# Optimization experiments

Measured on AMD Instinct MI355X. Metric: run time of the kernel, lower is better.

## Reference

```python
import jax, jax.numpy as jnp
import numpy as np

B, N, CI, CO, K = 4, 4096, 32, 32, 3


def setup_inputs() -> dict:
    key = jax.random.key(0)
    ks = jax.random.split(key, 28)
    f32 = jnp.float32

    def g(k, shape, scale=1.0):
        return jax.random.normal(k, shape, dtype=f32) * scale

    X = g(ks[0], (B, N, CI))
    L = g(ks[1], (N, N), 1.0 / np.sqrt(N))  # scaled Laplacian surrogate
    H = g(ks[2], (B, N, CO))
    C = g(ks[3], (B, N, CO))

    def conv_params(kw, ci):
        s = (2.0 / (ci + CO)) ** 0.5  # glorot-ish
        return g(kw, (K, ci, CO), s), jnp.zeros((CO,), f32)

    Wxi, bxi = conv_params(ks[4], CI)
    Whi, bhi = conv_params(ks[5], CO)
    Wxf, bxf = conv_params(ks[6], CI)
    Whf, bhf = conv_params(ks[7], CO)
    Wxc, bxc = conv_params(ks[8], CI)
    Whc, bhc = conv_params(ks[9], CO)
    Wxo, bxo = conv_params(ks[10], CI)
    Who, bho = conv_params(ks[11], CO)

    gs = (2.0 / (1 + CO)) ** 0.5
    w_ci = g(ks[12], (1, CO), gs)
    w_cf = g(ks[13], (1, CO), gs)
    w_co = g(ks[14], (1, CO), gs)
    b_i = jnp.zeros((1, CO), f32)
    b_f = jnp.zeros((1, CO), f32)
    b_c = jnp.zeros((1, CO), f32)
    b_o = jnp.zeros((1, CO), f32)

    return dict(X=X, L=L, H=H, C=C,
                Wxi=Wxi, bxi=bxi, Whi=Whi, bhi=bhi,
                Wxf=Wxf, bxf=bxf, Whf=Whf, bhf=bhf,
                Wxc=Wxc, bxc=bxc, Whc=Whc, bhc=bhc,
                Wxo=Wxo, bxo=bxo, Who=Who, bho=bho,
                w_ci=w_ci, w_cf=w_cf, w_co=w_co,
                b_i=b_i, b_f=b_f, b_c=b_c, b_o=b_o)


def cheb_conv(x, L, W, b):
    """Chebyshev graph conv: sum_k T_k(L) @ x @ W[k] + b.
    x: [B,N,F_in], L: [N,N], W: [K,F_in,F_out]."""
    Tx_prev = x                                    # T_0 = x
    out = jnp.einsum('bnf,fo->bno', Tx_prev, W[0])
    if W.shape[0] > 1:
        Tx = jnp.einsum('nm,bmf->bnf', L, x)       # T_1 = L x
        out = out + jnp.einsum('bnf,fo->bno', Tx, W[1])
        for k in range(2, W.shape[0]):
            Tx, Tx_prev = 2.0 * jnp.einsum('nm,bmf->bnf', L, Tx) - Tx_prev, Tx
            out = out + jnp.einsum('bnf,fo->bno', Tx, W[k])
    return out + b


def reference(X, L, H, C,
              Wxi, bxi, Whi, bhi,
              Wxf, bxf, Whf, bhf,
              Wxc, bxc, Whc, bhc,
              Wxo, bxo, Who, bho,
              w_ci, w_cf, w_co, b_i, b_f, b_c, b_o):
    I = jax.nn.sigmoid(cheb_conv(X, L, Wxi, bxi) + cheb_conv(H, L, Whi, bhi)
                       + w_ci * C + b_i)
    F = jax.nn.sigmoid(cheb_conv(X, L, Wxf, bxf) + cheb_conv(H, L, Whf, bhf)
                       + w_cf * C + b_f)
    T = jnp.tanh(cheb_conv(X, L, Wxc, bxc) + cheb_conv(H, L, Whc, bhc) + b_c)
    C_new = F * C + I * T
    O = jax.nn.sigmoid(cheb_conv(X, L, Wxo, bxo) + cheb_conv(H, L, Who, bho)
                       + w_co * C_new + b_o)
    H_new = O * jnp.tanh(C_new)
    return H_new, C_new
```

## Files before the change

### kernel.cpp

```cpp
#include <hip/hip_runtime.h>


typedef __bf16 bf16x8 __attribute__((ext_vector_type(8)));
typedef float f32x4 __attribute__((ext_vector_type(4)));

typedef unsigned short u16;
typedef unsigned int u32;

__device__ __forceinline__ float b2f(u16 h) {
  u32 u = ((u32)h) << 16;
  return __builtin_bit_cast(float, u);
}
__device__ __forceinline__ u16 f2b(float f) {
  u32 u = __builtin_bit_cast(u32, f);
  u += 0x7fffu + ((u >> 16) & 1u);
  return (u16)(u >> 16);
}
__device__ __forceinline__ u16 scrub16(u16 h) {
  return ((u16)(h & 0x7fffu) > (u16)0x7f80u) ? (u16)0 : h;
}
__device__ __forceinline__ float scrubf(float f) { return (f == f) ? f : 0.0f; }
__device__ __forceinline__ float sigm(float x) { return 1.0f / (1.0f + __expf(-x)); }
__device__ __forceinline__ float tanh_f(float x) { return 1.0f - 2.0f / (__expf(2.0f * x) + 1.0f); }

#define AS1 __attribute__((address_space(1)))
#define AS3 __attribute__((address_space(3)))
__device__ __forceinline__ void ld_lds16(const void* g, void* l) {
  __builtin_amdgcn_global_load_lds((const AS1 void*)g, (AS3 void*)l, 16, 0, 0);
}

#define FWS_M0T   0u
#define FWS_Y1T   2097152u
#define FWS_Y1N   4194304u
#define FWS_WCAT  6291456u
#define FWS_GB    6340608u
#define FWS_WC    6341120u
#define FWS_FLAG  6341632u
#define FWS_LBF   8388608u
#define FWS_PART  41943040u
#define FWS_TOTAL 58720256u
#define BWS_M0T   0u
#define BWS_Y1T   2097152u
#define BWS_Y1N   4194304u
#define BWS_T2N   6291456u
#define BWS_WCAT  8388608u
#define BWS_GB    8437760u
#define BWS_WC    8438272u
#define BWS_FLAG  8438784u

__global__ __launch_bounds__(64) void flag_k(const u16* __restrict__ L,
                                             u32* __restrict__ flag) {
  __shared__ int cnt;
  if (threadIdx.x == 0) cnt = 0;
  __syncthreads();
  int c = 0;
  for (int i = threadIdx.x; i < 1024; i += 64) {
    int e = (L[i] >> 7) & 0xFF;
    if (e >= 96 && e <= 126) ++c;
  }
  atomicAdd(&cnt, c);
  __syncthreads();
  if (threadIdx.x == 0) *flag = (cnt < 870) ? 1u : 0u;
}

__global__ __launch_bounds__(256) void convL_k(const void* __restrict__ L,
                                               u16* __restrict__ Lbf,
                                               const u32* __restrict__ flag) {
  const u32 mode = *flag;
  const int gtid = blockIdx.x * 256 + threadIdx.x;
  #pragma unroll
  for (int it = 0; it < 8; ++it) {
    const size_t e0 = ((size_t)it * 524288 + gtid) * 4;
    if (mode) {
      f32x4 v = *(const f32x4*)((const float*)L + e0);
      u16 o[4] = {f2b(v[0]), f2b(v[1]), f2b(v[2]), f2b(v[3])};
      *(uint2*)(Lbf + e0) = *(const uint2*)o;
    } else {
      *(uint2*)(Lbf + e0) = *(const uint2*)((const u16*)L + e0);
    }
  }
}

struct PackArgs {
  const void* in[27];
  u16* m0t;
  u16* wcat;
  float* gb;
  float* wc;
  const u32* flag;
};

__device__ __forceinline__ float rd_elem(const void* p, size_t idx, u32 mode) {
  return mode ? ((const float*)p)[idx] : b2f(((const u16*)p)[idx]);
}

__global__ __launch_bounds__(256) void pack_k(PackArgs pa) {
  const int bid = blockIdx.x;
  const int t = threadIdx.x;
  const u32 mode = *pa.flag;
  __shared__ u32 lds[256][17];

  if (bid < 128) {
    const int ts = bid >> 4, nc = bid & 15;
    const int xh = ts >> 2, b = ts & 3;
    const void* src = pa.in[xh ? 2 : 0];
    const int node = nc * 256 + t;
    const size_t rbase = ((size_t)b * 4096 + node) * 32;
    if (mode) {
      const f32x4* s4 = (const f32x4*)((const float*)src + rbase);
      u16 tv[32];
      #pragma unroll
      for (int j = 0; j < 8; ++j) {
        f32x4 v = s4[j];
        tv[j * 4] = f2b(v[0]); tv[j * 4 + 1] = f2b(v[1]);
        tv[j * 4 + 2] = f2b(v[2]); tv[j * 4 + 3] = f2b(v[3]);
      }
      #pragma unroll
      for (int i = 0; i < 16; ++i)
        lds[t][i] = (u32)tv[2 * i] | ((u32)tv[2 * i + 1] << 16);
    } else {
      const uint4* s4 = (const uint4*)((const u16*)src + rbase);
      uint4 q0 = s4[0], q1 = s4[1], q2 = s4[2], q3 = s4[3];
      lds[t][0] = q0.x;  lds[t][1] = q0.y;  lds[t][2] = q0.z;  lds[t][3] = q0.w;
      lds[t][4] = q1.x;  lds[t][5] = q1.y;  lds[t][6] = q1.z;  lds[t][7] = q1.w;
      lds[t][8] = q2.x;  lds[t][9] = q2.y;  lds[t][10] = q2.z; lds[t][11] = q2.w;
      lds[t][12] = q3.x; lds[t][13] = q3.y; lds[t][14] = q3.z; lds[t][15] = q3.w;
    }
    __syncthreads();
    const int f = t & 31, sc = t >> 5;
    const int ccol = xh * 128 + b * 32 + f;
    u16 tmp[32];
    #pragma unroll
    for (int i = 0; i < 32; ++i) {
      u32 wv = lds[sc * 32 + i][f >> 1];
      tmp[i] = scrub16((f & 1) ? (u16)(wv >> 16) : (u16)(wv & 0xffffu));
    }
    u16* dst = pa.m0t + (size_t)ccol * 4096 + nc * 256 + sc * 32;
    #pragma unroll
    for (int i = 0; i < 32; i += 8)
      *(uint4*)&dst[i] = *(const uint4*)&tmp[i];
  } else if (bid < 224) {
    const int wxi[4] = {4, 8, 12, 16};
    const int whi[4] = {6, 10, 14, 18};
    const int e = (bid - 128) * 256 + t;
    const int col = e / 192, j = e % 192;
    const int g = col >> 5, o = col & 31;
    const int a = j >> 5, jj = j & 31;
    const void* Wsrc = (a < 3) ? pa.in[wxi[g]] : pa.in[whi[g]];
    const int k = (a < 3) ? a : (a - 3);
    pa.wcat[e] = scrub16(f2b(rd_elem(Wsrc, k * 1024 + jj * 32 + o, mode)));
  } else {
    if (t < 128) {
      const int bx[4] = {5, 9, 13, 17}, bh[4] = {7, 11, 15, 19}, bb[4] = {23, 24, 25, 26};
      int g = t >> 5, o = t & 31;
      pa.gb[t] = scrubf(rd_elem(pa.in[bx[g]], o, mode) + rd_elem(pa.in[bh[g]], o, mode) +
                        rd_elem(pa.in[bb[g]], o, mode));
    } else if (t < 224) {
      int j = t - 128;
      int which = j >> 5, o = j & 31;
      pa.wc[j] = scrubf(rd_elem(pa.in[20 + which], o, mode));
    }
  }
}

__global__ __launch_bounds__(256, 4) void gemm_k(const u16* __restrict__ A,
                                                 const u16* __restrict__ B,
                                                 float* __restrict__ P) {
  __shared__ __align__(16) u16 ldsA[64 * 64];
  __shared__ __align__(16) u16 ldsB[64 * 64];
  const int tid = threadIdx.x;
  const int l = tid & 63;
  const int w = tid >> 6;
  const int rowTile = blockIdx.x & 63;
  const int colTile = (blockIdx.x >> 6) & 3;
  const int split = blockIdx.x >> 8;
  const int wRow = w >> 1, wCol = w & 1;

  f32x4 acc[4];
  #pragma unroll
  for (int i = 0; i < 4; ++i)
    #pragma unroll
    for (int e = 0; e < 4; ++e) acc[i][e] = 0.0f;

  const u16* Abase = A + (size_t)(rowTile * 64) * 4096 + split * 1024;
  const u16* Bbase = B + (size_t)(colTile * 64) * 4096 + split * 1024;

  const int lrow = l >> 3;
  const int gchunk = (l & 7) ^ lrow;

  for (int it = 0; it < 16; ++it) {
    const int kOff = it * 64;
    #pragma unroll
    for (int j = 0; j < 2; ++j) {
      const int rbase = w * 16 + j * 8;
      const int r = rbase + lrow;
      ld_lds16(Abase + (size_t)r * 4096 + kOff + gchunk * 8,
               &ldsA[rbase * 64 + l * 8]);
      ld_lds16(Bbase + (size_t)r * 4096 + kOff + gchunk * 8,
               &ldsB[rbase * 64 + l * 8]);
    }
    __syncthreads();
    #pragma unroll
    for (int kstep = 0; kstep < 2; ++kstep) {
      const int cg = kstep * 4 + (l >> 4);
      bf16x8 af[2], bf[2];
      #pragma unroll
      for (int mt = 0; mt < 2; ++mt) {
        const int m = wRow * 32 + mt * 16 + (l & 15);
        af[mt] = *(const bf16x8*)&ldsA[m * 64 + (cg ^ (m & 7)) * 8];
      }
      #pragma unroll
      for (int nt = 0; nt < 2; ++nt) {
        const int n = wCol * 32 + nt * 16 + (l & 15);
        bf[nt] = *(const bf16x8*)&ldsB[n * 64 + (cg ^ (n & 7)) * 8];
      }
      #pragma unroll
      for (int mt = 0; mt < 2; ++mt)
        #pragma unroll
        for (int nt = 0; nt < 2; ++nt)
          acc[mt * 2 + nt] =
              __builtin_amdgcn_mfma_f32_16x16x32_bf16(af[mt], bf[nt], acc[mt * 2 + nt], 0, 0, 0);
    }
    __syncthreads();
  }

  float* Pb = P + (size_t)split * 1048576;
  #pragma unroll
  for (int mt = 0; mt < 2; ++mt) {
    const int mBase = rowTile * 64 + wRow * 32 + mt * 16 + (l >> 4) * 4;
    #pragma unroll
    for (int nt = 0; nt < 2; ++nt) {
      const int c = colTile * 64 + wCol * 32 + nt * 16 + (l & 15);
      f32x4 v = acc[mt * 2 + nt];
      #pragma unroll
      for (int reg = 0; reg < 4; ++reg)
        Pb[(size_t)(mBase + reg) * 256 + c] = v[reg];
    }
  }
}

__global__ __launch_bounds__(256) void reduce_k(const float* __restrict__ P,
                                                u16* __restrict__ Y1T,
                                                u16* __restrict__ Y1N) {
  __shared__ __align__(16) u16 lds[16][264];
  const int t = threadIdx.x;
  const int n0 = blockIdx.x * 16;
  const int nl = t >> 4;
  const int n = n0 + nl;
  const int cb = (t & 15) * 16;
  u16 outv[16];
  #pragma unroll
  for (int cc = 0; cc < 16; cc += 4) {
    const float* p0 = P + (size_t)n * 256 + cb + cc;
    f32x4 s = *(const f32x4*)p0;
    s += *(const f32x4*)(p0 + 1048576);
    s += *(const f32x4*)(p0 + 2 * 1048576);
    s += *(const f32x4*)(p0 + 3 * 1048576);
    outv[cc] = f2b(s[0]); outv[cc + 1] = f2b(s[1]);
    outv[cc + 2] = f2b(s[2]); outv[cc + 3] = f2b(s[3]);
  }
  #pragma unroll
  for (int cc = 0; cc < 16; cc += 8) {
    *(uint4*)&Y1N[(size_t)n * 256 + cb + cc] = *(const uint4*)&outv[cc];
    *(uint4*)&lds[nl][cb + cc] = *(const uint4*)&outv[cc];
  }
  __syncthreads();
  const int c = t;
  u16 col[16];
  #pragma unroll
  for (int i = 0; i < 16; ++i) col[i] = lds[i][c];
  #pragma unroll
  for (int i = 0; i < 16; i += 8)
    *(uint4*)&Y1T[(size_t)c * 4096 + n0 + i] = *(const uint4*)&col[i];
}

struct CombArgs {
  const void* X; const void* H; const void* C;
  const u16* Y1N; const float* P;
  const u16* WCAT; const float* GB; const float* WC;
  void* OUT;
  const u32* flag;
};

__global__ __launch_bounds__(256) void combine_k(CombArgs a) {
  __shared__ __align__(16) u16 feat[64][200];
  const int t = threadIdx.x;
  const int l = t & 63;
  const int w = t >> 6;
  const int R0 = blockIdx.x * 64;
  const u32 mode = *a.flag;

  {
    const int R = R0 + l;
    const int b = R >> 12, n = R & 4095;
    if (w == 0) {
      if (mode) {
        const f32x4* xs = (const f32x4*)((const float*)a.X + (size_t)R * 32);
        const f32x4* hs = (const f32x4*)((const float*)a.H + (size_t)R * 32);
        u16 tx[32], th[32];
        #pragma unroll
        for (int j = 0; j < 8; ++j) {
          f32x4 vx = xs[j], vh = hs[j];
          tx[j * 4] = f2b(vx[0]); tx[j * 4 + 1] = f2b(vx[1]);
          tx[j * 4 + 2] = f2b(vx[2]); tx[j * 4 + 3] = f2b(vx[3]);
          th[j * 4] = f2b(vh[0]); th[j * 4 + 1] = f2b(vh[1]);
          th[j * 4 + 2] = f2b(vh[2]); th[j * 4 + 3] = f2b(vh[3]);
        }
        #pragma unroll
        for (int i = 0; i < 32; i += 8) {
          *(uint4*)&feat[l][i] = *(const uint4*)&tx[i];
          *(uint4*)&feat[l][96 + i] = *(const uint4*)&th[i];
        }
      } else {
        const uint4* xs = (const uint4*)((const u16*)a.X + (size_t)R * 32);
        *(uint4*)&feat[l][0] = xs[0];  *(uint4*)&feat[l][8] = xs[1];
        *(uint4*)&feat[l][16] = xs[2]; *(uint4*)&feat[l][24] = xs[3];
        const uint4* hs = (const uint4*)((const u16*)a.H + (size_t)R * 32);
        *(uint4*)&feat[l][96] = hs[0];  *(uint4*)&feat[l][104] = hs[1];
        *(uint4*)&feat[l][112] = hs[2]; *(uint4*)&feat[l][120] = hs[3];
      }
    } else if (w == 1) {
      const uint4* t1 = (const uint4*)(a.Y1N + (size_t)n * 256 + b * 32);
      *(uint4*)&feat[l][32] = t1[0]; *(uint4*)&feat[l][40] = t1[1];
      *(uint4*)&feat[l][48] = t1[2]; *(uint4*)&feat[l][56] = t1[3];
      const uint4* t1h = (const uint4*)(a.Y1N + (size_t)n * 256 + 128 + b * 32);
      *(uint4*)&feat[l][128] = t1h[0]; *(uint4*)&feat[l][136] = t1h[1];
      *(uint4*)&feat[l][144] = t1h[2]; *(uint4*)&feat[l][152] = t1h[3];
    } else {
      const int cOff = (w == 2) ? b * 32 : 128 + b * 32;
      const void* subp = (w == 2) ? a.X : a.H;
      float s[32];
      #pragma unroll
      for (int i = 0; i < 32; ++i) s[i] = 0.0f;
      for (int sp = 0; sp < 4; ++sp) {
        const float* p = a.P + (size_t)sp * 1048576 + (size_t)n * 256 + cOff;
        #pragma unroll
        for (int i = 0; i < 32; i += 4) {
          f32x4 v = *(const f32x4*)(p + i);
          s[i] += v[0]; s[i + 1] += v[1]; s[i + 2] += v[2]; s[i + 3] += v[3];
        }
      }
      u16 outv[32];
      #pragma unroll
      for (int i = 0; i < 32; ++i) {
        const float t0 = rd_elem(subp, (size_t)R * 32 + i, mode);
        outv[i] = f2b(2.0f * s[i] - t0);
      }
      const int seg = (w == 2) ? 64 : 160;
      #pragma unroll
      for (int i = 0; i < 32; i += 8)
        *(uint4*)&feat[l][seg + i] = *(const uint4*)&outv[i];
    }
  }
  __syncthreads();

  f32x4 acc[8];
  #pragma unroll
  for (int i = 0; i < 8; ++i)
    #pragma unroll
    for (int e = 0; e < 4; ++e) acc[i][e] = 0.0f;

  const int rowB = w * 16;
  #pragma unroll
  for (int ks = 0; ks < 6; ++ks) {
    bf16x8 af = *(const bf16x8*)&feat[rowB + (l & 15)][(l >> 4) * 8 + ks * 32];
    #pragma unroll
    for (int ct = 0; ct < 8; ++ct) {
      int ncol = ct * 16 + (l & 15);
      bf16x8 bv = *(const bf16x8*)&a.WCAT[(size_t)ncol * 192 + (l >> 4) * 8 + ks * 32];
      acc[ct] = __builtin_amdgcn_mfma_f32_16x16x32_bf16(af, bv, acc[ct], 0, 0, 0);
    }
  }

  const int o16 = l & 15;
  const int rq = (l >> 4) * 4;
  #pragma unroll
  for (int ctp = 0; ctp < 2; ++ctp) {
    const int o = ctp * 16 + o16;
    const float gbI = a.GB[o], gbF = a.GB[32 + o], gbT = a.GB[64 + o], gbO = a.GB[96 + o];
    const float wci = a.WC[o], wcf = a.WC[32 + o], wco = a.WC[64 + o];
    #pragma unroll
    for (int i = 0; i < 4; ++i) {
      const int R = R0 + w * 16 + rq + i;
      const size_t oidx = (size_t)R * 32 + o;
      const float cold = rd_elem(a.C, oidx, mode);
      const float vI = acc[0 + ctp][i] + gbI + wci * cold;
      const float vF = acc[2 + ctp][i] + gbF + wcf * cold;
      const float vT = acc[4 + ctp][i] + gbT;
      const float vO = acc[6 + ctp][i] + gbO;
      const float I = sigm(vI);
      const float F = sigm(vF);
      const float T = tanh_f(vT);
      const float Cn = F * cold + I * T;
      const float O = sigm(vO + wco * Cn);
      const float Hn = O * tanh_f(Cn);
      if (mode) {
        ((float*)a.OUT)[oidx] = Hn;
        ((float*)a.OUT)[524288 + oidx] = Cn;
      } else {
        ((u16*)a.OUT)[oidx] = f2b(Hn);
        ((u16*)a.OUT)[524288 + oidx] = f2b(Cn);
      }
    }
  }
}

#define LDS_STRIDE 72

__global__ __launch_bounds__(256) void gemm_fb(const void* __restrict__ A,
                                               const u16* __restrict__ B,
                                               const u16* __restrict__ M0T,
                                               u16* __restrict__ outN,
                                               u16* __restrict__ outT,
                                               const u32* __restrict__ flag,
                                               const int emode) {
  __shared__ __align__(16) u16 ldsA[64 * LDS_STRIDE];
  __shared__ __align__(16) u16 ldsB[64 * LDS_STRIDE];
  const int tid = threadIdx.x;
  const int l = tid & 63;
  const int w = tid >> 6;
  const int colTile = blockIdx.x & 3;
  const int rowTile = blockIdx.x >> 2;
  const int wRow = w >> 1, wCol = w & 1;
  const u32 mode = *flag;

  f32x4 acc[4];
  #pragma unroll
  for (int i = 0; i < 4; ++i)
    #pragma unroll
    for (int e = 0; e < 4; ++e) acc[i][e] = 0.0f;

  const size_t Aoff = (size_t)(rowTile * 64) * 4096;
  const u16* Bbase = B + (size_t)(colTile * 64) * 4096;

  const int srow = tid >> 2;
  const int sch = (tid & 3) * 2;

  for (int it = 0; it < 64; ++it) {
    const int kOff = it * 64;
    const size_t aidx = Aoff + (size_t)srow * 4096 + kOff + sch * 8;
    if (mode) {
      const float* Af = (const float*)A + aidx;
      u16 tv[16];
      #pragma unroll
      for (int q = 0; q < 4; ++q) {
        f32x4 v = *(const f32x4*)(Af + q * 4);
        tv[q * 4] = f2b(v[0]); tv[q * 4 + 1] = f2b(v[1]);
        tv[q * 4 + 2] = f2b(v[2]); tv[q * 4 + 3] = f2b(v[3]);
      }
      *(uint4*)&ldsA[srow * LDS_STRIDE + sch * 8] = ((const uint4*)tv)[0];
      *(uint4*)&ldsA[srow * LDS_STRIDE + sch * 8 + 8] = ((const uint4*)tv)[1];
    } else {
      const u16* ga = (const u16*)A + aidx;
      *(uint4*)&ldsA[srow * LDS_STRIDE + sch * 8] = *(const uint4*)ga;
      *(uint4*)&ldsA[srow * LDS_STRIDE + sch * 8 + 8] = *(const uint4*)(ga + 8);
    }
    const u16* gb = Bbase + (size_t)srow * 4096 + kOff + sch * 8;
    *(uint4*)&ldsB[srow * LDS_STRIDE + sch * 8] = *(const uint4*)gb;
    *(uint4*)&ldsB[srow * LDS_STRIDE + sch * 8 + 8] = *(const uint4*)(gb + 8);
    __syncthreads();
    #pragma unroll
    for (int kstep = 0; kstep < 2; ++kstep) {
      const int kb = kstep * 32 + (l >> 4) * 8;
      bf16x8 af[2], bf[2];
      #pragma unroll
      for (int mt = 0; mt < 2; ++mt)
        af[mt] = *(const bf16x8*)&ldsA[(wRow * 32 + mt * 16 + (l & 15)) * LDS_STRIDE + kb];
      #pragma unroll
      for (int nt = 0; nt < 2; ++nt)
        bf[nt] = *(const bf16x8*)&ldsB[(wCol * 32 + nt * 16 + (l & 15)) * LDS_STRIDE + kb];
      #pragma unroll
      for (int mt = 0; mt < 2; ++mt)
        #pragma unroll
        for (int nt = 0; nt < 2; ++nt)
          acc[mt * 2 + nt] =
              __builtin_amdgcn_mfma_f32_16x16x32_bf16(af[mt], bf[nt], acc[mt * 2 + nt], 0, 0, 0);
    }
    __syncthreads();
  }

  if (emode == 0) {
    #pragma unroll
    for (int mt = 0; mt < 2; ++mt) {
      const int mBase = rowTile * 64 + wRow * 32 + mt * 16 + (l >> 4) * 4;
      #pragma unroll
      for (int nt = 0; nt < 2; ++nt) {
        const int c = colTile * 64 + wCol * 32 + nt * 16 + (l & 15);
        f32x4 v = acc[mt * 2 + nt];
        #pragma unroll
        for (int reg = 0; reg < 4; ++reg) {
          const int m = mBase + reg;
          const u16 h = f2b(v[reg]);
          outN[(size_t)m * 256 + c] = h;
          outT[(size_t)c * 4096 + m] = h;
        }
      }
    }
  } else {
    #pragma unroll
    for (int mt = 0; mt < 2; ++mt) {
      const int mBase = rowTile * 64 + wRow * 32 + mt * 16 + (l >> 4) * 4;
      #pragma unroll
      for (int nt = 0; nt < 2; ++nt) {
        const int c = colTile * 64 + wCol * 32 + nt * 16 + (l & 15);
        f32x4 v = acc[mt * 2 + nt];
        #pragma unroll
        for (int reg = 0; reg < 4; ++reg) {
          const int m = mBase + reg;
          const float t0 = b2f(M0T[(size_t)c * 4096 + m]);
          outN[(size_t)m * 256 + c] = f2b(2.0f * v[reg] - t0);
        }
      }
    }
  }
}

struct CombFbArgs {
  const void* X; const void* H; const void* C;
  const u16* Y1N; const u16* T2N;
  const u16* WCAT; const float* GB; const float* WC;
  void* OUT;
  const u32* flag;
};

__global__ __launch_bounds__(256) void combine_fb(CombFbArgs a) {
  __shared__ __align__(16) u16 feat[64][200];
  const int t = threadIdx.x;
  const int l = t & 63;
  const int w = t >> 6;
  const int R0 = blockIdx.x * 64;
  const u32 mode = *a.flag;

  {
    const int R = R0 + l;
    const int b = R >> 12, n = R & 4095;
    if (w == 0) {
      if (mode) {
        const f32x4* xs = (const f32x4*)((const float*)a.X + (size_t)R * 32);
        const f32x4* hs = (const f32x4*)((const float*)a.H + (size_t)R * 32);
        u16 tx[32], th[32];
        #pragma unroll
        for (int j = 0; j < 8; ++j) {
          f32x4 vx = xs[j], vh = hs[j];
          tx[j * 4] = f2b(vx[0]); tx[j * 4 + 1] = f2b(vx[1]);
          tx[j * 4 + 2] = f2b(vx[2]); tx[j * 4 + 3] = f2b(vx[3]);
          th[j * 4] = f2b(vh[0]); th[j * 4 + 1] = f2b(vh[1]);
          th[j * 4 + 2] = f2b(vh[2]); th[j * 4 + 3] = f2b(vh[3]);
        }
        #pragma unroll
        for (int i = 0; i < 32; i += 8) {
          *(uint4*)&feat[l][i] = *(const uint4*)&tx[i];
          *(uint4*)&feat[l][96 + i] = *(const uint4*)&th[i];
        }
      } else {
        const uint4* xs = (const uint4*)((const u16*)a.X + (size_t)R * 32);
        *(uint4*)&feat[l][0] = xs[0];  *(uint4*)&feat[l][8] = xs[1];
        *(uint4*)&feat[l][16] = xs[2]; *(uint4*)&feat[l][24] = xs[3];
        const uint4* hs = (const uint4*)((const u16*)a.H + (size_t)R * 32);
        *(uint4*)&feat[l][96] = hs[0];  *(uint4*)&feat[l][104] = hs[1];
        *(uint4*)&feat[l][112] = hs[2]; *(uint4*)&feat[l][120] = hs[3];
      }
    } else if (w == 1) {
      const uint4* t1 = (const uint4*)(a.Y1N + (size_t)n * 256 + b * 32);
      *(uint4*)&feat[l][32] = t1[0]; *(uint4*)&feat[l][40] = t1[1];
      *(uint4*)&feat[l][48] = t1[2]; *(uint4*)&feat[l][56] = t1[3];
      const uint4* t1h = (const uint4*)(a.Y1N + (size_t)n * 256 + 128 + b * 32);
      *(uint4*)&feat[l][128] = t1h[0]; *(uint4*)&feat[l][136] = t1h[1];
      *(uint4*)&feat[l][144] = t1h[2]; *(uint4*)&feat[l][152] = t1h[3];
    } else if (w == 2) {
      const uint4* t2 = (const uint4*)(a.T2N + (size_t)n * 256 + b * 32);
      *(uint4*)&feat[l][64] = t2[0]; *(uint4*)&feat[l][72] = t2[1];
      *(uint4*)&feat[l][80] = t2[2]; *(uint4*)&feat[l][88] = t2[3];
      const uint4* t2h = (const uint4*)(a.T2N + (size_t)n * 256 + 128 + b * 32);
      *(uint4*)&feat[l][160] = t2h[0]; *(uint4*)&feat[l][168] = t2h[1];
      *(uint4*)&feat[l][176] = t2h[2]; *(uint4*)&feat[l][184] = t2h[3];
    }
  }
  __syncthreads();

  f32x4 acc[8];
  #pragma unroll
  for (int i = 0; i < 8; ++i)
    #pragma unroll
    for (int e = 0; e < 4; ++e) acc[i][e] = 0.0f;

  const int rowB = w * 16;
  #pragma unroll
  for (int ks = 0; ks < 6; ++ks) {
    bf16x8 af = *(const bf16x8*)&feat[rowB + (l & 15)][(l >> 4) * 8 + ks * 32];
    #pragma unroll
    for (int ct = 0; ct < 8; ++ct) {
      int ncol = ct * 16 + (l & 15);
      bf16x8 bv = *(const bf16x8*)&a.WCAT[(size_t)ncol * 192 + (l >> 4) * 8 + ks * 32];
      acc[ct] = __builtin_amdgcn_mfma_f32_16x16x32_bf16(af, bv, acc[ct], 0, 0, 0);
    }
  }

  const int o16 = l & 15;
  const int rq = (l >> 4) * 4;
  #pragma unroll
  for (int ctp = 0; ctp < 2; ++ctp) {
    const int o = ctp * 16 + o16;
    const float gbI = a.GB[o], gbF = a.GB[32 + o], gbT = a.GB[64 + o], gbO = a.GB[96 + o];
    const float wci = a.WC[o], wcf = a.WC[32 + o], wco = a.WC[64 + o];
    #pragma unroll
    for (int i = 0; i < 4; ++i) {
      const int R = R0 + w * 16 + rq + i;
      const size_t oidx = (size_t)R * 32 + o;
      const float cold = rd_elem(a.C, oidx, mode);
      const float vI = acc[0 + ctp][i] + gbI + wci * cold;
      const float vF = acc[2 + ctp][i] + gbF + wcf * cold;
      const float vT = acc[4 + ctp][i] + gbT;
      const float vO = acc[6 + ctp][i] + gbO;
      const float I = sigm(vI);
      const float F = sigm(vF);
      const float T = tanh_f(vT);
      const float Cn = F * cold + I * T;
      const float O = sigm(vO + wco * Cn);
      const float Hn = O * tanh_f(Cn);
      if (mode) {
        ((float*)a.OUT)[oidx] = Hn;
        ((float*)a.OUT)[524288 + oidx] = Cn;
      } else {
        ((u16*)a.OUT)[oidx] = f2b(Hn);
        ((u16*)a.OUT)[524288 + oidx] = f2b(Cn);
      }
    }
  }
}

extern "C" void kernel_launch(void* const* d_in, const int* in_sizes, int n_in,
                              void* d_out, int out_size, void* d_ws, size_t ws_size,
                              hipStream_t stream) {
  char* ws = (char*)d_ws;
  const bool fast = ws_size >= (size_t)FWS_TOTAL;

  if (fast) {
    u16* M0T = (u16*)(ws + FWS_M0T);
    u16* Y1T = (u16*)(ws + FWS_Y1T);
    u16* Y1N = (u16*)(ws + FWS_Y1N);
    u16* WCAT = (u16*)(ws + FWS_WCAT);
    float* GB = (float*)(ws + FWS_GB);
    float* WC = (float*)(ws + FWS_WC);
    u32* FLAG = (u32*)(ws + FWS_FLAG);
    u16* LBF = (u16*)(ws + FWS_LBF);
    float* PART = (float*)(ws + FWS_PART);

    flag_k<<<1, 64, 0, stream>>>((const u16*)d_in[1], FLAG);
    convL_k<<<2048, 256, 0, stream>>>(d_in[1], LBF, FLAG);

    PackArgs pa;
    for (int i = 0; i < 27; ++i) pa.in[i] = d_in[i];
    pa.m0t = M0T; pa.wcat = WCAT; pa.gb = GB; pa.wc = WC; pa.flag = FLAG;
    pack_k<<<225, 256, 0, stream>>>(pa);

    gemm_k<<<1024, 256, 0, stream>>>(LBF, M0T, PART);
    reduce_k<<<256, 256, 0, stream>>>(PART, Y1T, Y1N);
    gemm_k<<<1024, 256, 0, stream>>>(LBF, Y1T, PART);

    CombArgs ca;
    ca.X = d_in[0]; ca.H = d_in[2]; ca.C = d_in[3];
    ca.Y1N = Y1N; ca.P = PART; ca.WCAT = WCAT; ca.GB = GB; ca.WC = WC;
    ca.OUT = d_out; ca.flag = FLAG;
    combine_k<<<256, 256, 0, stream>>>(ca);
  } else {
    u16* M0T = (u16*)(ws + BWS_M0T);
    u16* Y1T = (u16*)(ws + BWS_Y1T);
    u16* Y1N = (u16*)(ws + BWS_Y1N);
    u16* T2N = (u16*)(ws + BWS_T2N);
    u16* WCAT = (u16*)(ws + BWS_WCAT);
    float* GB = (float*)(ws + BWS_GB);
    float* WC = (float*)(ws + BWS_WC);
    u32* FLAG = (u32*)(ws + BWS_FLAG);

    flag_k<<<1, 64, 0, stream>>>((const u16*)d_in[1], FLAG);

    PackArgs pa;
    for (int i = 0; i < 27; ++i) pa.in[i] = d_in[i];
    pa.m0t = M0T; pa.wcat = WCAT; pa.gb = GB; pa.wc = WC; pa.flag = FLAG;
    pack_k<<<225, 256, 0, stream>>>(pa);

    gemm_fb<<<256, 256, 0, stream>>>(d_in[1], M0T, nullptr, Y1N, Y1T, FLAG, 0);
    gemm_fb<<<256, 256, 0, stream>>>(d_in[1], Y1T, M0T, T2N, nullptr, FLAG, 1);

    CombFbArgs ca;
    ca.X = d_in[0]; ca.H = d_in[2]; ca.C = d_in[3];
    ca.Y1N = Y1N; ca.T2N = T2N; ca.WCAT = WCAT; ca.GB = GB; ca.WC = WC;
    ca.OUT = d_out; ca.flag = FLAG;
    combine_fb<<<225 == 0 ? 1 : 256, 256, 0, stream>>>(ca);
  }
}
```

Before: 213.1 us.

## Widen GEMM tile to full output width with 8-way split-K and fuse mode detection

The L-GEMM now has each block compute a 64x256 output tile (16 accumulators per wave), so each L tile is loaded once instead of four times. K is split eight ways over 512 columns each; the reduce and combine kernels sum 8 partials. The separate flag kernel is removed: every convL block detects the input mode itself and block 0 writes the flag. The costs are more fp32 partial traffic, lower occupancy, and a larger workspace requirement that may push execution onto the fallback path.

```diff
diff --git a/kernel.cpp b/kernel.cpp
--- a/kernel.cpp
+++ b/kernel.cpp
@@ -38,7 +38,7 @@
 #define FWS_FLAG  6341632u
 #define FWS_LBF   8388608u
 #define FWS_PART  41943040u
-#define FWS_TOTAL 58720256u
+#define FWS_TOTAL 75497472u
 #define BWS_M0T   0u
 #define BWS_Y1T   2097152u
 #define BWS_Y1N   4194304u
@@ -48,25 +48,35 @@
 #define BWS_WC    8438272u
 #define BWS_FLAG  8438784u
 
-__global__ __launch_bounds__(64) void flag_k(const u16* __restrict__ L,
-                                             u32* __restrict__ flag) {
-  __shared__ int cnt;
-  if (threadIdx.x == 0) cnt = 0;
+__device__ __forceinline__ u32 detect_mode(const u16* __restrict__ L,
+                                           int* cntLds) {
+  const int t = threadIdx.x;
+  if (t == 0) *cntLds = 0;
   __syncthreads();
   int c = 0;
-  for (int i = threadIdx.x; i < 1024; i += 64) {
-    int e = (L[i] >> 7) & 0xFF;
-    if (e >= 96 && e <= 126) ++c;
-  }
-  atomicAdd(&cnt, c);
+  #pragma unroll
+  for (int i = 0; i < 4; ++i) {
+    int e = (L[t * 4 + i] >> 7) & 0xFF;
+    c += (e >= 96 && e <= 126) ? 1 : 0;
+  }
+  atomicAdd(cntLds, c);
   __syncthreads();
-  if (threadIdx.x == 0) *flag = (cnt < 870) ? 1u : 0u;
+  return (*cntLds < 870) ? 1u : 0u;
+}
+
+__global__ __launch_bounds__(256) void flag_k(const u16* __restrict__ L,
+                                              u32* __restrict__ flag) {
+  __shared__ int cnt;
+  u32 m = detect_mode(L, &cnt);
+  if (threadIdx.x == 0) *flag = m;
 }
 
 __global__ __launch_bounds__(256) void convL_k(const void* __restrict__ L,
                                                u16* __restrict__ Lbf,
-                                               const u32* __restrict__ flag) {
-  const u32 mode = *flag;
+                                               u32* __restrict__ flag) {
+  __shared__ int cnt;
+  const u32 mode = detect_mode((const u16*)L, &cnt);
+  if (blockIdx.x == 0 && threadIdx.x == 0) *flag = mode;
   const int gtid = blockIdx.x * 256 + threadIdx.x;
   #pragma unroll
   for (int it = 0; it < 8; ++it) {
@@ -163,32 +173,30 @@
   }
 }
 
-__global__ __launch_bounds__(256, 4) void gemm_k(const u16* __restrict__ A,
+__global__ __launch_bounds__(256, 2) void gemm_k(const u16* __restrict__ A,
                                                  const u16* __restrict__ B,
                                                  float* __restrict__ P) {
   __shared__ __align__(16) u16 ldsA[64 * 64];
-  __shared__ __align__(16) u16 ldsB[64 * 64];
+  __shared__ __align__(16) u16 ldsB[256 * 64];
   const int tid = threadIdx.x;
   const int l = tid & 63;
   const int w = tid >> 6;
   const int rowTile = blockIdx.x & 63;
-  const int colTile = (blockIdx.x >> 6) & 3;
-  const int split = blockIdx.x >> 8;
-  const int wRow = w >> 1, wCol = w & 1;
-
-  f32x4 acc[4];
-  #pragma unroll
-  for (int i = 0; i < 4; ++i)
+  const int split = blockIdx.x >> 6;
+
+  f32x4 acc[16];
+  #pragma unroll
+  for (int i = 0; i < 16; ++i)
     #pragma unroll
     for (int e = 0; e < 4; ++e) acc[i][e] = 0.0f;
 
-  const u16* Abase = A + (size_t)(rowTile * 64) * 4096 + split * 1024;
-  const u16* Bbase = B + (size_t)(colTile * 64) * 4096 + split * 1024;
+  const u16* Abase = A + (size_t)(rowTile * 64) * 4096 + split * 512;
+  const u16* Bbase = B + split * 512;
 
   const int lrow = l >> 3;
   const int gchunk = (l & 7) ^ lrow;
 
-  for (int it = 0; it < 16; ++it) {
+  for (int it = 0; it < 8; ++it) {
     const int kOff = it * 64;
     #pragma unroll
     for (int j = 0; j < 2; ++j) {
@@ -196,6 +204,11 @@
       const int r = rbase + lrow;
       ld_lds16(Abase + (size_t)r * 4096 + kOff + gchunk * 8,
                &ldsA[rbase * 64 + l * 8]);
+    }
+    #pragma unroll
+    for (int j = 0; j < 8; ++j) {
+      const int rbase = w * 64 + j * 8;
+      const int r = rbase + lrow;
       ld_lds16(Bbase + (size_t)r * 4096 + kOff + gchunk * 8,
                &ldsB[rbase * 64 + l * 8]);
     }
@@ -203,35 +216,35 @@
     #pragma unroll
     for (int kstep = 0; kstep < 2; ++kstep) {
       const int cg = kstep * 4 + (l >> 4);
-      bf16x8 af[2], bf[2];
-      #pragma unroll
-      for (int mt = 0; mt < 2; ++mt) {
-        const int m = wRow * 32 + mt * 16 + (l & 15);
+      bf16x8 af[4], bf[4];
+      #pragma unroll
+      for (int mt = 0; mt < 4; ++mt) {
+        const int m = mt * 16 + (l & 15);
         af[mt] = *(const bf16x8*)&ldsA[m * 64 + (cg ^ (m & 7)) * 8];
       }
       #pragma unroll
-      for (int nt = 0; nt < 2; ++nt) {
-        const int n = wCol * 32 + nt * 16 + (l & 15);
+      for (int nt = 0; nt < 4; ++nt) {
+        const int n = w * 64 + nt * 16 + (l & 15);
         bf[nt] = *(const bf16x8*)&ldsB[n * 64 + (cg ^ (n & 7)) * 8];
       }
       #pragma unroll
-      for (int mt = 0; mt < 2; ++mt)
-        #pragma unroll
-        for (int nt = 0; nt < 2; ++nt)
-          acc[mt * 2 + nt] =
-              __builtin_amdgcn_mfma_f32_16x16x32_bf16(af[mt], bf[nt], acc[mt * 2 + nt], 0, 0, 0);
+      for (int mt = 0; mt < 4; ++mt)
+        #pragma unroll
+        for (int nt = 0; nt < 4; ++nt)
+          acc[mt * 4 + nt] =
+              __builtin_amdgcn_mfma_f32_16x16x32_bf16(af[mt], bf[nt], acc[mt * 4 + nt], 0, 0, 0);
     }
     __syncthreads();
   }
 
   float* Pb = P + (size_t)split * 1048576;
   #pragma unroll
-  for (int mt = 0; mt < 2; ++mt) {
-    const int mBase = rowTile * 64 + wRow * 32 + mt * 16 + (l >> 4) * 4;
-    #pragma unroll
-    for (int nt = 0; nt < 2; ++nt) {
-      const int c = colTile * 64 + wCol * 32 + nt * 16 + (l & 15);
-      f32x4 v = acc[mt * 2 + nt];
+  for (int mt = 0; mt < 4; ++mt) {
+    const int mBase = rowTile * 64 + mt * 16 + (l >> 4) * 4;
+    #pragma unroll
+    for (int nt = 0; nt < 4; ++nt) {
+      const int c = w * 64 + nt * 16 + (l & 15);
+      f32x4 v = acc[mt * 4 + nt];
       #pragma unroll
       for (int reg = 0; reg < 4; ++reg)
         Pb[(size_t)(mBase + reg) * 256 + c] = v[reg];
@@ -253,9 +266,9 @@
   for (int cc = 0; cc < 16; cc += 4) {
     const float* p0 = P + (size_t)n * 256 + cb + cc;
     f32x4 s = *(const f32x4*)p0;
-    s += *(const f32x4*)(p0 + 1048576);
-    s += *(const f32x4*)(p0 + 2 * 1048576);
-    s += *(const f32x4*)(p0 + 3 * 1048576);
+    #pragma unroll
+    for (int sp = 1; sp < 8; ++sp)
+      s += *(const f32x4*)(p0 + (size_t)sp * 1048576);
     outv[cc] = f2b(s[0]); outv[cc + 1] = f2b(s[1]);
     outv[cc + 2] = f2b(s[2]); outv[cc + 3] = f2b(s[3]);
   }
@@ -332,7 +345,7 @@
       float s[32];
       #pragma unroll
       for (int i = 0; i < 32; ++i) s[i] = 0.0f;
-      for (int sp = 0; sp < 4; ++sp) {
+      for (int sp = 0; sp < 8; ++sp) {
         const float* p = a.P + (size_t)sp * 1048576 + (size_t)n * 256 + cOff;
         #pragma unroll
         for (int i = 0; i < 32; i += 4) {
@@ -646,7 +659,6 @@
     u16* LBF = (u16*)(ws + FWS_LBF);
     float* PART = (float*)(ws + FWS_PART);
 
-    flag_k<<<1, 64, 0, stream>>>((const u16*)d_in[1], FLAG);
     convL_k<<<2048, 256, 0, stream>>>(d_in[1], LBF, FLAG);
 
     PackArgs pa;
@@ -654,9 +666,9 @@
     pa.m0t = M0T; pa.wcat = WCAT; pa.gb = GB; pa.wc = WC; pa.flag = FLAG;
     pack_k<<<225, 256, 0, stream>>>(pa);
 
-    gemm_k<<<1024, 256, 0, stream>>>(LBF, M0T, PART);
+    gemm_k<<<512, 256, 0, stream>>>(LBF, M0T, PART);
     reduce_k<<<256, 256, 0, stream>>>(PART, Y1T, Y1N);
-    gemm_k<<<1024, 256, 0, stream>>>(LBF, Y1T, PART);
+    gemm_k<<<512, 256, 0, stream>>>(LBF, Y1T, PART);
 
     CombArgs ca;
     ca.X = d_in[0]; ca.H = d_in[2]; ca.C = d_in[3];
@@ -673,7 +685,7 @@
     float* WC = (float*)(ws + BWS_WC);
     u32* FLAG = (u32*)(ws + BWS_FLAG);
 
-    flag_k<<<1, 64, 0, stream>>>((const u16*)d_in[1], FLAG);
+    flag_k<<<1, 256, 0, stream>>>((const u16*)d_in[1], FLAG);
 
     PackArgs pa;
     for (int i = 0; i < 27; ++i) pa.in[i] = d_in[i];
@@ -687,6 +699,6 @@
     ca.X = d_in[0]; ca.H = d_in[2]; ca.C = d_in[3];
     ca.Y1N = Y1N; ca.T2N = T2N; ca.WCAT = WCAT; ca.GB = GB; ca.WC = WC;
     ca.OUT = d_out; ca.flag = FLAG;
-    combine_fb<<<225 == 0 ? 1 : 256, 256, 0, stream>>>(ca);
-  }
-}
+    combine_fb<<<256, 256, 0, stream>>>(ca);
+  }
+}
```

Measured after the change: 218.4 us. 1.02x slower.
